# Optimization experiments

Hardware: AMD Instinct MI355X
Metric: run time of the kernel (lower is better)

## Reference

```python
import jax, jax.numpy as jnp
import numpy as np

N_HEADS = 16

def kernel_sigmoid(x):
    return jax.nn.sigmoid(0.6053 * x - 4.102)

def setup_inputs() -> dict:
    key = jax.random.key(0)
    kq, kk, kv = jax.random.split(key, 3)
    B, LQ, LK, E = 4, 4096, 4096, 1024
    return {
        "Q": jax.random.normal(kq, (B, LQ, E), dtype=jnp.float32),
        "K": jax.random.normal(kk, (B, LK, E), dtype=jnp.float32),
        "V": jax.random.normal(kv, (B, LK, E), dtype=jnp.float32),
    }

def reference(Q, K, V):
    B, LQ, E = Q.shape
    LK = K.shape[1]
    H = N_HEADS
    D = E // H
    # split heads -> [B, H, L, D]
    Qh = Q.reshape(B, LQ, H, D).transpose(0, 2, 1, 3)
    Kh = K.reshape(B, LK, H, D).transpose(0, 2, 1, 3)
    Vh = V.reshape(B, LK, H, D).transpose(0, 2, 1, 3)
    phi_Q = kernel_sigmoid(Qh)           # [B,H,LQ,D]
    phi_K = kernel_sigmoid(Kh)           # [B,H,LK,D]
    # KV state: phi_K^T @ V -> [B,H,D,D]
    kv = jnp.einsum("bhkd,bhke->bhde", phi_K, Vh)
    num = jnp.einsum("bhqd,bhde->bhqe", phi_Q, kv)      # [B,H,LQ,D]
    k_sum = phi_K.sum(axis=2)                            # [B,H,D]
    den = jnp.einsum("bhqd,bhd->bhq", phi_Q, k_sum)      # [B,H,LQ]
    out = num / den[..., None]
    # merge heads -> [B, LQ, E]
    return out.transpose(0, 2, 1, 3).reshape(B, LQ, E)
```

## Files before the change

kernel.cpp:

```cpp
#include <hip/hip_runtime.h>
#include <cstdint>
#include <cstddef>

#define B_ 4
#define L_ 4096
#define E_ 1024
#define H_ 16
#define D_ 64
#define BH_ 64
#define ST2_ 4160
#define NCH_ 16
#define RPC_ (L_/NCH_)
#define NT_ (RPC_/32)

typedef __attribute__((ext_vector_type(8))) short short8v;
typedef __attribute__((ext_vector_type(4))) float f32x4;

__device__ __forceinline__ float sigk(float x) {
    return __builtin_amdgcn_rcpf(1.0f + __expf(4.102f - 0.6053f * x));
}
__device__ __forceinline__ unsigned short bfh(float f) {
    union { float f; unsigned u; } v; v.f = f;
    const unsigned r = v.u + 0x7fffu + ((v.u >> 16) & 1u);
    return (unsigned short)(r >> 16);
}
__device__ __forceinline__ float bf2f(unsigned short s) {
    union { unsigned u; float f; } v; v.u = ((unsigned)s) << 16;
    return v.f;
}


__global__ void __launch_bounds__(256) kv_partial_kernel(
    const float* __restrict__ K, const float* __restrict__ V,
    float* __restrict__ partial)
{
    __shared__ short8v Bfrag[2 * 8 * 64];

    const int ch = blockIdx.x & (NCH_ - 1);
    const int bh = blockIdx.x / NCH_;
    const int b = bh >> 4, h = bh & 15;
    const int tid = threadIdx.x;
    const int w = tid >> 6, l = tid & 63;
    const int g = l >> 4, m = l & 15;
    const int k4 = g << 2;
    const int col = (w << 4) + m;

    const float* Kp = K + (size_t)(b * L_ + ch * RPC_) * E_ + h * D_ + col;
    const float* Vp = V + (size_t)(b * L_ + ch * RPC_) * E_ + h * D_ + col;

    f32x4 acc[4];
    #pragma unroll
    for (int t = 0; t < 4; ++t) acc[t] = (f32x4){0.f, 0.f, 0.f, 0.f};
    float ksacc = 0.f;

    float vr[8], kr[8];
    #pragma unroll
    for (int j = 0; j < 8; ++j) {
        const int ko = k4 + (j & 3) + ((j >> 2) << 4);
        vr[j] = Vp[(size_t)ko * E_];
        kr[j] = Kp[(size_t)ko * E_];
    }
    {
        short8v Bh, Bl;
        #pragma unroll
        for (int j = 0; j < 8; ++j) {
            const unsigned short hb = bfh(vr[j]);
            Bh[j] = (short)hb;
            Bl[j] = (short)bfh(vr[j] - bf2f(hb));
        }
        Bfrag[(w << 1) * 64 + l]       = Bh;
        Bfrag[((w << 1) + 1) * 64 + l] = Bl;
    }
    __syncthreads();

    #pragma unroll 2
    for (int t = 0; t < NT_; ++t) {
        const int buf = (t & 1) << 9;
        float vr2[8], kr2[8];
        if (t + 1 < NT_) {
            #pragma unroll
            for (int j = 0; j < 8; ++j) {
                const int ko = ((t + 1) << 5) + k4 + (j & 3) + ((j >> 2) << 4);
                vr2[j] = Vp[(size_t)ko * E_];
                kr2[j] = Kp[(size_t)ko * E_];
            }
        }
        short8v Ah;
        #pragma unroll
        for (int j = 0; j < 8; ++j) {
            const unsigned short hb = bfh(sigk(kr[j]));
            Ah[j] = (short)hb;
            ksacc += bf2f(hb);
        }
        #pragma unroll
        for (int tt = 0; tt < 4; ++tt) {
            const short8v Bh = Bfrag[buf + (tt << 1) * 64 + l];
            const short8v Bl = Bfrag[buf + ((tt << 1) + 1) * 64 + l];
            acc[tt] = __builtin_amdgcn_mfma_f32_16x16x32_bf16(Ah, Bh, acc[tt], 0, 0, 0);
            acc[tt] = __builtin_amdgcn_mfma_f32_16x16x32_bf16(Ah, Bl, acc[tt], 0, 0, 0);
        }
        if (t + 1 < NT_) {
            const int nbuf = ((t + 1) & 1) << 9;
            short8v Bh, Bl;
            #pragma unroll
            for (int j = 0; j < 8; ++j) {
                const unsigned short hb = bfh(vr2[j]);
                Bh[j] = (short)hb;
                Bl[j] = (short)bfh(vr2[j] - bf2f(hb));
            }
            Bfrag[nbuf + (w << 1) * 64 + l]       = Bh;
            Bfrag[nbuf + ((w << 1) + 1) * 64 + l] = Bl;
            #pragma unroll
            for (int j = 0; j < 8; ++j) kr[j] = kr2[j];
        }
        __syncthreads();
    }

    ksacc += __shfl_xor(ksacc, 16);
    ksacc += __shfl_xor(ksacc, 32);

    const size_t pbase = ((size_t)ch * BH_ + bh) * ST2_;
    #pragma unroll
    for (int tt = 0; tt < 4; ++tt)
        #pragma unroll
        for (int r = 0; r < 4; ++r)
            partial[pbase + (size_t)((w << 4) + k4 + r) * 64 + (tt << 4) + m]
                = acc[tt][r];
    if (g == 0) partial[pbase + 4096 + (w << 4) + m] = ksacc;
}

__global__ void __launch_bounds__(256) kv_reduce_kernel(
    const float* __restrict__ partial, unsigned* __restrict__ kv2,
    float* __restrict__ ksumf)
{
    const int bh = blockIdx.x >> 2, part = blockIdx.x & 3;
    const int tid = threadIdx.x;
    #pragma unroll
    for (int i = 0; i < 4; ++i) {
        const int idx = (part << 10) + (i << 8) + tid;
        float s = 0.f;
        #pragma unroll
        for (int c = 0; c < NCH_; ++c)
            s += partial[((size_t)c * BH_ + bh) * ST2_ + idx];
        const unsigned short hb = bfh(s);
        const unsigned short lb = bfh(s - bf2f(hb));
        kv2[(size_t)bh * 4096 + idx] = ((unsigned)hb << 16) | (unsigned)lb;
    }
    if (part == 0 && tid < 64) {
        float s = 0.f;
        #pragma unroll
        for (int c = 0; c < NCH_; ++c)
            s += partial[((size_t)c * BH_ + bh) * ST2_ + 4096 + tid];
        ksumf[bh * 64 + tid] = s;
    }
}

__global__ void __launch_bounds__(256) attn_out_kernel(
    const float* __restrict__ Q, const unsigned* __restrict__ kv2,
    const float* __restrict__ ksumf, float* __restrict__ out)
{
    __shared__ short8v fragBv[16 * 64];
    __shared__ float Qt[64 * 65];
    unsigned short* fragB = (unsigned short*)fragBv;

    const int bh = blockIdx.x >> 5, qb = blockIdx.x & 31;
    const int b = bh >> 4, h = bh & 15;
    const int tid = threadIdx.x;
    const int w = tid >> 6, l = tid & 63;
    const int g = l >> 4, m = l & 15;
    const int k4 = g << 2;

    #pragma unroll 4
    for (int i = 0; i < 16; ++i) {
        const int idx = tid + (i << 8);
        const unsigned u = kv2[(size_t)bh * 4096 + idx];
        const int dd = idx >> 6, e = idx & 63;
        const int kk = dd & 31, kstep = dd >> 5;
        const int gg = (kk & 15) >> 2;
        const int jj = (kk & 3) + ((kk >> 4) << 2);
        const int lane = (e & 15) + (gg << 4);
        const int tt2 = e >> 4;
        const int slot = (((kstep << 2) + tt2) << 1);
        fragB[(slot * 64 + lane) * 8 + jj]       = (unsigned short)(u >> 16);
        fragB[((slot + 1) * 64 + lane) * 8 + jj] = (unsigned short)(u & 0xffffu);
    }
    float ksl[16];
    #pragma unroll
    for (int ks = 0; ks < 2; ++ks)
        #pragma unroll
        for (int j = 0; j < 8; ++j)
            ksl[ks * 8 + j] =
                ksumf[bh * 64 + (ks << 5) + k4 + (j & 3) + ((j >> 2) << 4)];
    __syncthreads();

    for (int qt = 0; qt < 2; ++qt) {
        const int rowb0 = (qb << 7) + (qt << 6);
        #pragma unroll
        for (int i = 0; i < 4; ++i) {
            const int idx = tid + (i << 8);
            const int r = idx >> 4, c4i = (idx & 15) << 2;
            const float4 qv = *(const float4*)(
                Q + (size_t)(b * L_ + rowb0 + r) * E_ + h * D_ + c4i);
            float* qd = Qt + r * 65 + c4i;
            qd[0] = qv.x; qd[1] = qv.y; qd[2] = qv.z; qd[3] = qv.w;
        }
        __syncthreads();

        const int rl = (w << 4) + m;
        short8v Ah[2], Al[2];
        float den = 0.f;
        #pragma unroll
        for (int ks = 0; ks < 2; ++ks)
            #pragma unroll
            for (int j = 0; j < 8; ++j) {
                const float qv =
                    Qt[rl * 65 + (ks << 5) + k4 + (j & 3) + ((j >> 2) << 4)];
                const float ph = sigk(qv);
                const unsigned short hb = bfh(ph);
                Ah[ks][j] = (short)hb;
                Al[ks][j] = (short)bfh(ph - bf2f(hb));
                den = fmaf(ph, ksl[ks * 8 + j], den);
            }

        f32x4 acc[4];
        #pragma unroll
        for (int tt = 0; tt < 4; ++tt) acc[tt] = (f32x4){0.f, 0.f, 0.f, 0.f};
        #pragma unroll
        for (int ks = 0; ks < 2; ++ks)
            #pragma unroll
            for (int tt = 0; tt < 4; ++tt) {
                const int slot = (((ks << 2) + tt) << 1);
                const short8v Bh = fragBv[slot * 64 + l];
                const short8v Bl = fragBv[(slot + 1) * 64 + l];
                acc[tt] = __builtin_amdgcn_mfma_f32_16x16x32_bf16(Ah[ks], Bh, acc[tt], 0, 0, 0);
                acc[tt] = __builtin_amdgcn_mfma_f32_16x16x32_bf16(Ah[ks], Bl, acc[tt], 0, 0, 0);
                acc[tt] = __builtin_amdgcn_mfma_f32_16x16x32_bf16(Al[ks], Bh, acc[tt], 0, 0, 0);
            }

        den += __shfl_xor(den, 16);
        den += __shfl_xor(den, 32);
        float inv[4];
        #pragma unroll
        for (int r = 0; r < 4; ++r)
            inv[r] = __builtin_amdgcn_rcpf(__shfl(den, k4 + r));

        float* op = out + (size_t)(b * L_ + rowb0 + (w << 4)) * E_ + h * D_;
        #pragma unroll
        for (int tt = 0; tt < 4; ++tt)
            #pragma unroll
            for (int r = 0; r < 4; ++r)
                op[(size_t)(k4 + r) * E_ + (tt << 4) + m] = acc[tt][r] * inv[r];
        __syncthreads();
    }
}

extern "C" void kernel_launch(void* const* d_in, const int* in_sizes, int n_in,
                              void* d_out, int out_size, void* d_ws, size_t ws_size,
                              hipStream_t stream) {
    const float* Q = (const float*)d_in[0];
    const float* K = (const float*)d_in[1];
    const float* V = (const float*)d_in[2];
    float* out = (float*)d_out;

    float* partial  = (float*)d_ws;
    unsigned* kv2   = (unsigned*)(partial + (size_t)NCH_ * BH_ * ST2_);
    float* ksumf    = (float*)(kv2 + (size_t)BH_ * 4096);

    hipLaunchKernelGGL(kv_partial_kernel, dim3(BH_ * NCH_), dim3(256), 0, stream,
                       K, V, partial);
    hipLaunchKernelGGL(kv_reduce_kernel, dim3(BH_ * 4), dim3(256), 0, stream,
                       partial, kv2, ksumf);
    hipLaunchKernelGGL(attn_out_kernel, dim3(BH_ * 32), dim3(256), 0, stream,
                       Q, kv2, ksumf, out);
}
```

Before: 69.82 us.

## Raise KV chunk count, pre-swizzle KV fragments, one Q tile per block

The KV partial pass now splits each head into a runtime-chosen chunk count, up to 32 and capped by workspace size, to raise parallelism. The reduce kernel writes the hi/lo bf16 KV state directly in MFMA fragment order, so the output kernel can copy it into LDS with plain loads. The output kernel handles one 64-row Q tile per block with twice as many blocks, and precomputes the sigmoid and bf16 split of Q while staging it. The costs are more partial traffic in the reduce and more redundant KV staging across the extra output blocks.

```diff
diff --git a/kernel.cpp b/kernel.cpp
--- a/kernel.cpp
+++ b/kernel.cpp
@@ -9,9 +9,6 @@
 #define D_ 64
 #define BH_ 64
 #define ST2_ 4160
-#define NCH_ 16
-#define RPC_ (L_/NCH_)
-#define NT_ (RPC_/32)
 
 typedef __attribute__((ext_vector_type(8))) short short8v;
 typedef __attribute__((ext_vector_type(4))) float f32x4;
@@ -32,12 +29,12 @@
 
 __global__ void __launch_bounds__(256) kv_partial_kernel(
     const float* __restrict__ K, const float* __restrict__ V,
-    float* __restrict__ partial)
+    float* __restrict__ partial, int nch, int rowsPerCh, int nt)
 {
     __shared__ short8v Bfrag[2 * 8 * 64];
 
-    const int ch = blockIdx.x & (NCH_ - 1);
-    const int bh = blockIdx.x / NCH_;
+    const int ch = blockIdx.x % nch;
+    const int bh = blockIdx.x / nch;
     const int b = bh >> 4, h = bh & 15;
     const int tid = threadIdx.x;
     const int w = tid >> 6, l = tid & 63;
@@ -45,8 +42,8 @@
     const int k4 = g << 2;
     const int col = (w << 4) + m;
 
-    const float* Kp = K + (size_t)(b * L_ + ch * RPC_) * E_ + h * D_ + col;
-    const float* Vp = V + (size_t)(b * L_ + ch * RPC_) * E_ + h * D_ + col;
+    const float* Kp = K + (size_t)(b * L_ + ch * rowsPerCh) * E_ + h * D_ + col;
+    const float* Vp = V + (size_t)(b * L_ + ch * rowsPerCh) * E_ + h * D_ + col;
 
     f32x4 acc[4];
     #pragma unroll
@@ -74,10 +71,10 @@
     __syncthreads();
 
     #pragma unroll 2
-    for (int t = 0; t < NT_; ++t) {
+    for (int t = 0; t < nt; ++t) {
         const int buf = (t & 1) << 9;
         float vr2[8], kr2[8];
-        if (t + 1 < NT_) {
+        if (t + 1 < nt) {
             #pragma unroll
             for (int j = 0; j < 8; ++j) {
                 const int ko = ((t + 1) << 5) + k4 + (j & 3) + ((j >> 2) << 4);
@@ -99,7 +96,7 @@
             acc[tt] = __builtin_amdgcn_mfma_f32_16x16x32_bf16(Ah, Bh, acc[tt], 0, 0, 0);
             acc[tt] = __builtin_amdgcn_mfma_f32_16x16x32_bf16(Ah, Bl, acc[tt], 0, 0, 0);
         }
-        if (t + 1 < NT_) {
+        if (t + 1 < nt) {
             const int nbuf = ((t + 1) & 1) << 9;
             short8v Bh, Bl;
             #pragma unroll
@@ -131,7 +128,7 @@
 
 __global__ void __launch_bounds__(256) kv_reduce_kernel(
     const float* __restrict__ partial, unsigned* __restrict__ kv2,
-    float* __restrict__ ksumf)
+    float* __restrict__ ksumf, int nch)
 {
     const int bh = blockIdx.x >> 2, part = blockIdx.x & 3;
     const int tid = threadIdx.x;
@@ -139,17 +136,22 @@
     for (int i = 0; i < 4; ++i) {
         const int idx = (part << 10) + (i << 8) + tid;
         float s = 0.f;
-        #pragma unroll
-        for (int c = 0; c < NCH_; ++c)
+        for (int c = 0; c < nch; ++c)
             s += partial[((size_t)c * BH_ + bh) * ST2_ + idx];
         const unsigned short hb = bfh(s);
         const unsigned short lb = bfh(s - bf2f(hb));
-        kv2[(size_t)bh * 4096 + idx] = ((unsigned)hb << 16) | (unsigned)lb;
+        const unsigned u = ((unsigned)hb << 16) | (unsigned)lb;
+        const int d = idx >> 6, e = idx & 63;
+        const int kk = d & 31;
+        const int gg = (kk & 15) >> 2;
+        const int jj = (kk & 3) + ((kk >> 4) << 2);
+        const int lane = (e & 15) + (gg << 4);
+        const int sp = ((d >> 5) << 2) + (e >> 4);
+        kv2[(size_t)bh * 4096 + ((sp << 6) + lane) * 8 + jj] = u;
     }
     if (part == 0 && tid < 64) {
         float s = 0.f;
-        #pragma unroll
-        for (int c = 0; c < NCH_; ++c)
+        for (int c = 0; c < nch; ++c)
             s += partial[((size_t)c * BH_ + bh) * ST2_ + 4096 + tid];
         ksumf[bh * 64 + tid] = s;
     }
@@ -159,99 +161,106 @@
     const float* __restrict__ Q, const unsigned* __restrict__ kv2,
     const float* __restrict__ ksumf, float* __restrict__ out)
 {
-    __shared__ short8v fragBv[16 * 64];
-    __shared__ float Qt[64 * 65];
-    unsigned short* fragB = (unsigned short*)fragBv;
-
-    const int bh = blockIdx.x >> 5, qb = blockIdx.x & 31;
+    __shared__ unsigned kvf[4096];
+    __shared__ uint4 QA4[1024];
+
+    const int bh = blockIdx.x >> 6, qb = blockIdx.x & 63;
     const int b = bh >> 4, h = bh & 15;
     const int tid = threadIdx.x;
     const int w = tid >> 6, l = tid & 63;
     const int g = l >> 4, m = l & 15;
     const int k4 = g << 2;
-
-    #pragma unroll 4
-    for (int i = 0; i < 16; ++i) {
+    const int rowb0 = qb << 6;
+
+    #pragma unroll
+    for (int i = 0; i < 16; ++i)
+        kvf[tid + (i << 8)] = kv2[(size_t)bh * 4096 + tid + (i << 8)];
+
+    #pragma unroll
+    for (int i = 0; i < 4; ++i) {
         const int idx = tid + (i << 8);
-        const unsigned u = kv2[(size_t)bh * 4096 + idx];
-        const int dd = idx >> 6, e = idx & 63;
-        const int kk = dd & 31, kstep = dd >> 5;
-        const int gg = (kk & 15) >> 2;
-        const int jj = (kk & 3) + ((kk >> 4) << 2);
-        const int lane = (e & 15) + (gg << 4);
-        const int tt2 = e >> 4;
-        const int slot = (((kstep << 2) + tt2) << 1);
-        fragB[(slot * 64 + lane) * 8 + jj]       = (unsigned short)(u >> 16);
-        fragB[((slot + 1) * 64 + lane) * 8 + jj] = (unsigned short)(u & 0xffffu);
-    }
+        const int r = idx >> 4;
+        const int c4i = (idx & 15) << 2;
+        const float4 qv = *(const float4*)(
+            Q + (size_t)(b * L_ + rowb0 + r) * E_ + h * D_ + c4i);
+        const float qa[4] = {qv.x, qv.y, qv.z, qv.w};
+        unsigned u[4];
+        #pragma unroll
+        for (int j = 0; j < 4; ++j) {
+            const float ph = sigk(qa[j]);
+            const unsigned short hb = bfh(ph);
+            const unsigned short lb = bfh(ph - bf2f(hb));
+            u[j] = ((unsigned)hb << 16) | (unsigned)lb;
+        }
+        const int lane = (tid >> 4) + ((tid & 3) << 4);
+        const int qq = (tid >> 2) & 3;
+        QA4[(((qq << 2) + i) << 6) + lane] = make_uint4(u[0], u[1], u[2], u[3]);
+    }
+
     float ksl[16];
     #pragma unroll
+    for (int ji = 0; ji < 16; ++ji) {
+        const int ks = ji >> 3, j = ji & 7;
+        ksl[ji] = ksumf[bh * 64 + (ks << 5) + k4 + (j & 3) + ((j >> 2) << 4)];
+    }
+    __syncthreads();
+
+    const uint4 aq0 = QA4[((0 << 2) + w) * 64 + l];
+    const uint4 aq1 = QA4[((1 << 2) + w) * 64 + l];
+    const uint4 aq2 = QA4[((2 << 2) + w) * 64 + l];
+    const uint4 aq3 = QA4[((3 << 2) + w) * 64 + l];
+    const unsigned au[16] = {aq0.x, aq0.y, aq0.z, aq0.w,
+                             aq1.x, aq1.y, aq1.z, aq1.w,
+                             aq2.x, aq2.y, aq2.z, aq2.w,
+                             aq3.x, aq3.y, aq3.z, aq3.w};
+    short8v Ah[2], Al[2];
+    float den = 0.f;
+    #pragma unroll
+    for (int ji = 0; ji < 16; ++ji) {
+        const unsigned uu = au[ji];
+        const unsigned short hb = (unsigned short)(uu >> 16);
+        const unsigned short lb = (unsigned short)(uu & 0xffffu);
+        Ah[ji >> 3][ji & 7] = (short)hb;
+        Al[ji >> 3][ji & 7] = (short)lb;
+        den = fmaf(bf2f(hb) + bf2f(lb), ksl[ji], den);
+    }
+
+    f32x4 acc[4];
+    #pragma unroll
+    for (int tt = 0; tt < 4; ++tt) acc[tt] = (f32x4){0.f, 0.f, 0.f, 0.f};
+    #pragma unroll
     for (int ks = 0; ks < 2; ++ks)
         #pragma unroll
-        for (int j = 0; j < 8; ++j)
-            ksl[ks * 8 + j] =
-                ksumf[bh * 64 + (ks << 5) + k4 + (j & 3) + ((j >> 2) << 4)];
-    __syncthreads();
-
-    for (int qt = 0; qt < 2; ++qt) {
-        const int rowb0 = (qb << 7) + (qt << 6);
-        #pragma unroll
-        for (int i = 0; i < 4; ++i) {
-            const int idx = tid + (i << 8);
-            const int r = idx >> 4, c4i = (idx & 15) << 2;
-            const float4 qv = *(const float4*)(
-                Q + (size_t)(b * L_ + rowb0 + r) * E_ + h * D_ + c4i);
-            float* qd = Qt + r * 65 + c4i;
-            qd[0] = qv.x; qd[1] = qv.y; qd[2] = qv.z; qd[3] = qv.w;
-        }
-        __syncthreads();
-
-        const int rl = (w << 4) + m;
-        short8v Ah[2], Al[2];
-        float den = 0.f;
-        #pragma unroll
-        for (int ks = 0; ks < 2; ++ks)
+        for (int tt = 0; tt < 4; ++tt) {
+            const int base = ((((ks << 2) + tt) << 6) + l) << 3;
+            const uint4 b0 = *(const uint4*)&kvf[base];
+            const uint4 b1 = *(const uint4*)&kvf[base + 4];
+            const unsigned bu[8] = {b0.x, b0.y, b0.z, b0.w,
+                                    b1.x, b1.y, b1.z, b1.w};
+            short8v Bh, Bl;
             #pragma unroll
             for (int j = 0; j < 8; ++j) {
-                const float qv =
-                    Qt[rl * 65 + (ks << 5) + k4 + (j & 3) + ((j >> 2) << 4)];
-                const float ph = sigk(qv);
-                const unsigned short hb = bfh(ph);
-                Ah[ks][j] = (short)hb;
-                Al[ks][j] = (short)bfh(ph - bf2f(hb));
-                den = fmaf(ph, ksl[ks * 8 + j], den);
+                Bh[j] = (short)(bu[j] >> 16);
+                Bl[j] = (short)(bu[j] & 0xffffu);
             }
-
-        f32x4 acc[4];
-        #pragma unroll
-        for (int tt = 0; tt < 4; ++tt) acc[tt] = (f32x4){0.f, 0.f, 0.f, 0.f};
-        #pragma unroll
-        for (int ks = 0; ks < 2; ++ks)
-            #pragma unroll
-            for (int tt = 0; tt < 4; ++tt) {
-                const int slot = (((ks << 2) + tt) << 1);
-                const short8v Bh = fragBv[slot * 64 + l];
-                const short8v Bl = fragBv[(slot + 1) * 64 + l];
-                acc[tt] = __builtin_amdgcn_mfma_f32_16x16x32_bf16(Ah[ks], Bh, acc[tt], 0, 0, 0);
-                acc[tt] = __builtin_amdgcn_mfma_f32_16x16x32_bf16(Ah[ks], Bl, acc[tt], 0, 0, 0);
-                acc[tt] = __builtin_amdgcn_mfma_f32_16x16x32_bf16(Al[ks], Bh, acc[tt], 0, 0, 0);
-            }
-
-        den += __shfl_xor(den, 16);
-        den += __shfl_xor(den, 32);
-        float inv[4];
+            acc[tt] = __builtin_amdgcn_mfma_f32_16x16x32_bf16(Ah[ks], Bh, acc[tt], 0, 0, 0);
+            acc[tt] = __builtin_amdgcn_mfma_f32_16x16x32_bf16(Ah[ks], Bl, acc[tt], 0, 0, 0);
+            acc[tt] = __builtin_amdgcn_mfma_f32_16x16x32_bf16(Al[ks], Bh, acc[tt], 0, 0, 0);
+        }
+
+    den += __shfl_xor(den, 16);
+    den += __shfl_xor(den, 32);
+    float inv[4];
+    #pragma unroll
+    for (int r = 0; r < 4; ++r)
+        inv[r] = __builtin_amdgcn_rcpf(__shfl(den, k4 + r));
+
+    float* op = out + (size_t)(b * L_ + rowb0 + (w << 4)) * E_ + h * D_;
+    #pragma unroll
+    for (int tt = 0; tt < 4; ++tt)
         #pragma unroll
         for (int r = 0; r < 4; ++r)
-            inv[r] = __builtin_amdgcn_rcpf(__shfl(den, k4 + r));
-
-        float* op = out + (size_t)(b * L_ + rowb0 + (w << 4)) * E_ + h * D_;
-        #pragma unroll
-        for (int tt = 0; tt < 4; ++tt)
-            #pragma unroll
-            for (int r = 0; r < 4; ++r)
-                op[(size_t)(k4 + r) * E_ + (tt << 4) + m] = acc[tt][r] * inv[r];
-        __syncthreads();
-    }
+            op[(size_t)(k4 + r) * E_ + (tt << 4) + m] = acc[tt][r] * inv[r];
 }
 
 extern "C" void kernel_launch(void* const* d_in, const int* in_sizes, int n_in,
@@ -262,14 +271,22 @@
     const float* V = (const float*)d_in[2];
     float* out = (float*)d_out;
 
+    int nch = 32;
+    while (nch > 4 &&
+           (size_t)nch * BH_ * ST2_ * 4 + (size_t)BH_ * 4096 * 4 + BH_ * 64 * 4
+               > ws_size)
+        nch >>= 1;
+    const int rowsPerCh = L_ / nch;
+    const int nt = rowsPerCh / 32;
+
     float* partial  = (float*)d_ws;
-    unsigned* kv2   = (unsigned*)(partial + (size_t)NCH_ * BH_ * ST2_);
+    unsigned* kv2   = (unsigned*)(partial + (size_t)nch * BH_ * ST2_);
     float* ksumf    = (float*)(kv2 + (size_t)BH_ * 4096);
 
-    hipLaunchKernelGGL(kv_partial_kernel, dim3(BH_ * NCH_), dim3(256), 0, stream,
-                       K, V, partial);
+    hipLaunchKernelGGL(kv_partial_kernel, dim3(BH_ * nch), dim3(256), 0, stream,
+                       K, V, partial, nch, rowsPerCh, nt);
     hipLaunchKernelGGL(kv_reduce_kernel, dim3(BH_ * 4), dim3(256), 0, stream,
-                       partial, kv2, ksumf);
-    hipLaunchKernelGGL(attn_out_kernel, dim3(BH_ * 32), dim3(256), 0, stream,
+                       partial, kv2, ksumf, nch);
+    hipLaunchKernelGGL(attn_out_kernel, dim3(BH_ * 64), dim3(256), 0, stream,
                        Q, kv2, ksumf, out);
 }
```

Result: slower. 110.6 us (+58.5%).

## Pre-swizzle KV state into MFMA fragment layout and deepen K/V prefetch

Applied to the files above, without the earlier changes.

The reduce kernel now writes the KV state as separate hi/lo bf16 arrays already arranged in MFMA B-fragment order. The output kernel can then copy it to shared memory with straight vector loads instead of a scattered 16-bit shuffle. The output kernel handles one 64-row query tile per block with twice as many blocks, which removes its loop and the extra barriers. The partial kernel prefetches K/V two tiles ahead and adds a scheduling barrier. The denominator now uses the bf16-split phi value, and the extra register and register-to-shared traffic may add pressure.

```diff
diff --git a/kernel.cpp b/kernel.cpp
--- a/kernel.cpp
+++ b/kernel.cpp
@@ -53,65 +53,72 @@
     for (int t = 0; t < 4; ++t) acc[t] = (f32x4){0.f, 0.f, 0.f, 0.f};
     float ksacc = 0.f;
 
-    float vr[8], kr[8];
+    float kr[2][8], vr[2][8];
     #pragma unroll
     for (int j = 0; j < 8; ++j) {
         const int ko = k4 + (j & 3) + ((j >> 2) << 4);
-        vr[j] = Vp[(size_t)ko * E_];
-        kr[j] = Kp[(size_t)ko * E_];
+        kr[0][j] = Kp[(size_t)ko * E_];
+        vr[0][j] = Vp[(size_t)ko * E_];
     }
     {
         short8v Bh, Bl;
         #pragma unroll
         for (int j = 0; j < 8; ++j) {
-            const unsigned short hb = bfh(vr[j]);
+            const unsigned short hb = bfh(vr[0][j]);
             Bh[j] = (short)hb;
-            Bl[j] = (short)bfh(vr[j] - bf2f(hb));
+            Bl[j] = (short)bfh(vr[0][j] - bf2f(hb));
         }
         Bfrag[(w << 1) * 64 + l]       = Bh;
         Bfrag[((w << 1) + 1) * 64 + l] = Bl;
     }
+    #pragma unroll
+    for (int j = 0; j < 8; ++j) {
+        const int ko = 32 + k4 + (j & 3) + ((j >> 2) << 4);
+        kr[1][j] = Kp[(size_t)ko * E_];
+        vr[1][j] = Vp[(size_t)ko * E_];
+    }
     __syncthreads();
 
     #pragma unroll 2
     for (int t = 0; t < NT_; ++t) {
-        const int buf = (t & 1) << 9;
-        float vr2[8], kr2[8];
-        if (t + 1 < NT_) {
+        const int cur = t & 1, nxt = cur ^ 1;
+        short8v Ah;
+        #pragma unroll
+        for (int j = 0; j < 8; ++j) {
+            const unsigned short hb = bfh(sigk(kr[cur][j]));
+            Ah[j] = (short)hb;
+            ksacc += bf2f(hb);
+        }
+        if (t + 2 < NT_) {
             #pragma unroll
             for (int j = 0; j < 8; ++j) {
-                const int ko = ((t + 1) << 5) + k4 + (j & 3) + ((j >> 2) << 4);
-                vr2[j] = Vp[(size_t)ko * E_];
-                kr2[j] = Kp[(size_t)ko * E_];
+                const int ko = ((t + 2) << 5) + k4 + (j & 3) + ((j >> 2) << 4);
+                kr[cur][j] = Kp[(size_t)ko * E_];
+                vr[cur][j] = Vp[(size_t)ko * E_];
             }
         }
-        short8v Ah;
-        #pragma unroll
-        for (int j = 0; j < 8; ++j) {
-            const unsigned short hb = bfh(sigk(kr[j]));
-            Ah[j] = (short)hb;
-            ksacc += bf2f(hb);
-        }
-        #pragma unroll
-        for (int tt = 0; tt < 4; ++tt) {
-            const short8v Bh = Bfrag[buf + (tt << 1) * 64 + l];
-            const short8v Bl = Bfrag[buf + ((tt << 1) + 1) * 64 + l];
-            acc[tt] = __builtin_amdgcn_mfma_f32_16x16x32_bf16(Ah, Bh, acc[tt], 0, 0, 0);
-            acc[tt] = __builtin_amdgcn_mfma_f32_16x16x32_bf16(Ah, Bl, acc[tt], 0, 0, 0);
+        __builtin_amdgcn_sched_barrier(0);
+        {
+            const int buf = cur << 9;
+            #pragma unroll
+            for (int tt = 0; tt < 4; ++tt) {
+                const short8v Bh = Bfrag[buf + (tt << 1) * 64 + l];
+                const short8v Bl = Bfrag[buf + ((tt << 1) + 1) * 64 + l];
+                acc[tt] = __builtin_amdgcn_mfma_f32_16x16x32_bf16(Ah, Bh, acc[tt], 0, 0, 0);
+                acc[tt] = __builtin_amdgcn_mfma_f32_16x16x32_bf16(Ah, Bl, acc[tt], 0, 0, 0);
+            }
         }
         if (t + 1 < NT_) {
-            const int nbuf = ((t + 1) & 1) << 9;
+            const int nb = nxt << 9;
             short8v Bh, Bl;
             #pragma unroll
             for (int j = 0; j < 8; ++j) {
-                const unsigned short hb = bfh(vr2[j]);
+                const unsigned short hb = bfh(vr[nxt][j]);
                 Bh[j] = (short)hb;
-                Bl[j] = (short)bfh(vr2[j] - bf2f(hb));
+                Bl[j] = (short)bfh(vr[nxt][j] - bf2f(hb));
             }
-            Bfrag[nbuf + (w << 1) * 64 + l]       = Bh;
-            Bfrag[nbuf + ((w << 1) + 1) * 64 + l] = Bl;
-            #pragma unroll
-            for (int j = 0; j < 8; ++j) kr[j] = kr2[j];
+            Bfrag[nb + (w << 1) * 64 + l]       = Bh;
+            Bfrag[nb + ((w << 1) + 1) * 64 + l] = Bl;
         }
         __syncthreads();
     }
@@ -130,21 +137,34 @@
 }
 
 __global__ void __launch_bounds__(256) kv_reduce_kernel(
-    const float* __restrict__ partial, unsigned* __restrict__ kv2,
-    float* __restrict__ ksumf)
+    const float* __restrict__ partial, unsigned* __restrict__ kv2H,
+    unsigned* __restrict__ kv2L, float* __restrict__ ksumf)
 {
     const int bh = blockIdx.x >> 2, part = blockIdx.x & 3;
     const int tid = threadIdx.x;
-    #pragma unroll
-    for (int i = 0; i < 4; ++i) {
-        const int idx = (part << 10) + (i << 8) + tid;
-        float s = 0.f;
-        #pragma unroll
-        for (int c = 0; c < NCH_; ++c)
-            s += partial[((size_t)c * BH_ + bh) * ST2_ + idx];
-        const unsigned short hb = bfh(s);
-        const unsigned short lb = bfh(s - bf2f(hb));
-        kv2[(size_t)bh * 4096 + idx] = ((unsigned)hb << 16) | (unsigned)lb;
+    const int e = tid & 63;
+    #pragma unroll
+    for (int it = 0; it < 2; ++it) {
+        const int pr = (tid >> 6) + (it << 2);
+        const int d0 = (part << 4) + (pr << 1);
+        float s0 = 0.f, s1 = 0.f;
+        #pragma unroll
+        for (int c = 0; c < NCH_; ++c) {
+            const size_t pb = ((size_t)c * BH_ + bh) * ST2_;
+            s0 += partial[pb + (d0 << 6) + e];
+            s1 += partial[pb + ((d0 + 1) << 6) + e];
+        }
+        const unsigned short h0 = bfh(s0), h1 = bfh(s1);
+        const unsigned short l0 = bfh(s0 - bf2f(h0));
+        const unsigned short l1 = bfh(s1 - bf2f(h1));
+        const int kk = d0 & 31;
+        const int gg = (kk & 15) >> 2;
+        const int jq = ((kk & 3) >> 1) + ((kk >> 4) << 1);
+        const int lane = (e & 15) + (gg << 4);
+        const int sp = ((d0 >> 5) << 2) + (e >> 4);
+        const size_t idx = (size_t)bh * 2048 + (((sp << 6) + lane) << 2) + jq;
+        kv2H[idx] = (unsigned)h0 | ((unsigned)h1 << 16);
+        kv2L[idx] = (unsigned)l0 | ((unsigned)l1 << 16);
     }
     if (part == 0 && tid < 64) {
         float s = 0.f;
@@ -156,102 +176,94 @@
 }
 
 __global__ void __launch_bounds__(256) attn_out_kernel(
-    const float* __restrict__ Q, const unsigned* __restrict__ kv2,
-    const float* __restrict__ ksumf, float* __restrict__ out)
+    const float* __restrict__ Q, const unsigned* __restrict__ kv2H,
+    const unsigned* __restrict__ kv2L, const float* __restrict__ ksumf,
+    float* __restrict__ out)
 {
-    __shared__ short8v fragBv[16 * 64];
+    __shared__ short8v kvH[8 * 64];
+    __shared__ short8v kvL[8 * 64];
     __shared__ float Qt[64 * 65];
-    unsigned short* fragB = (unsigned short*)fragBv;
-
-    const int bh = blockIdx.x >> 5, qb = blockIdx.x & 31;
+
+    const int bh = blockIdx.x >> 6, qb = blockIdx.x & 63;
     const int b = bh >> 4, h = bh & 15;
     const int tid = threadIdx.x;
     const int w = tid >> 6, l = tid & 63;
     const int g = l >> 4, m = l & 15;
     const int k4 = g << 2;
-
-    #pragma unroll 4
-    for (int i = 0; i < 16; ++i) {
+    const int rowb0 = qb << 6;
+
+    {
+        const uint4* srcH = (const uint4*)(kv2H + (size_t)bh * 2048);
+        const uint4* srcL = (const uint4*)(kv2L + (size_t)bh * 2048);
+        uint4* dH = (uint4*)kvH;
+        uint4* dL = (uint4*)kvL;
+        dH[tid]       = srcH[tid];
+        dH[tid + 256] = srcH[tid + 256];
+        dL[tid]       = srcL[tid];
+        dL[tid + 256] = srcL[tid + 256];
+    }
+    #pragma unroll
+    for (int i = 0; i < 4; ++i) {
         const int idx = tid + (i << 8);
-        const unsigned u = kv2[(size_t)bh * 4096 + idx];
-        const int dd = idx >> 6, e = idx & 63;
-        const int kk = dd & 31, kstep = dd >> 5;
-        const int gg = (kk & 15) >> 2;
-        const int jj = (kk & 3) + ((kk >> 4) << 2);
-        const int lane = (e & 15) + (gg << 4);
-        const int tt2 = e >> 4;
-        const int slot = (((kstep << 2) + tt2) << 1);
-        fragB[(slot * 64 + lane) * 8 + jj]       = (unsigned short)(u >> 16);
-        fragB[((slot + 1) * 64 + lane) * 8 + jj] = (unsigned short)(u & 0xffffu);
+        const int r = idx >> 4, c4i = (idx & 15) << 2;
+        const float4 qv = *(const float4*)(
+            Q + (size_t)(b * L_ + rowb0 + r) * E_ + h * D_ + c4i);
+        float* qd = Qt + r * 65 + c4i;
+        qd[0] = qv.x; qd[1] = qv.y; qd[2] = qv.z; qd[3] = qv.w;
     }
     float ksl[16];
     #pragma unroll
+    for (int ji = 0; ji < 16; ++ji) {
+        const int ks = ji >> 3, j = ji & 7;
+        ksl[ji] = ksumf[bh * 64 + (ks << 5) + k4 + (j & 3) + ((j >> 2) << 4)];
+    }
+    __syncthreads();
+
+    const int rl = (w << 4) + m;
+    short8v Ah[2], Al[2];
+    float den = 0.f;
+    #pragma unroll
     for (int ks = 0; ks < 2; ++ks)
         #pragma unroll
-        for (int j = 0; j < 8; ++j)
-            ksl[ks * 8 + j] =
-                ksumf[bh * 64 + (ks << 5) + k4 + (j & 3) + ((j >> 2) << 4)];
-    __syncthreads();
-
-    for (int qt = 0; qt < 2; ++qt) {
-        const int rowb0 = (qb << 7) + (qt << 6);
-        #pragma unroll
-        for (int i = 0; i < 4; ++i) {
-            const int idx = tid + (i << 8);
-            const int r = idx >> 4, c4i = (idx & 15) << 2;
-            const float4 qv = *(const float4*)(
-                Q + (size_t)(b * L_ + rowb0 + r) * E_ + h * D_ + c4i);
-            float* qd = Qt + r * 65 + c4i;
-            qd[0] = qv.x; qd[1] = qv.y; qd[2] = qv.z; qd[3] = qv.w;
-        }
-        __syncthreads();
-
-        const int rl = (w << 4) + m;
-        short8v Ah[2], Al[2];
-        float den = 0.f;
-        #pragma unroll
-        for (int ks = 0; ks < 2; ++ks)
-            #pragma unroll
-            for (int j = 0; j < 8; ++j) {
-                const float qv =
-                    Qt[rl * 65 + (ks << 5) + k4 + (j & 3) + ((j >> 2) << 4)];
-                const float ph = sigk(qv);
-                const unsigned short hb = bfh(ph);
-                Ah[ks][j] = (short)hb;
-                Al[ks][j] = (short)bfh(ph - bf2f(hb));
-                den = fmaf(ph, ksl[ks * 8 + j], den);
-            }
-
-        f32x4 acc[4];
-        #pragma unroll
-        for (int tt = 0; tt < 4; ++tt) acc[tt] = (f32x4){0.f, 0.f, 0.f, 0.f};
-        #pragma unroll
-        for (int ks = 0; ks < 2; ++ks)
-            #pragma unroll
-            for (int tt = 0; tt < 4; ++tt) {
-                const int slot = (((ks << 2) + tt) << 1);
-                const short8v Bh = fragBv[slot * 64 + l];
-                const short8v Bl = fragBv[(slot + 1) * 64 + l];
-                acc[tt] = __builtin_amdgcn_mfma_f32_16x16x32_bf16(Ah[ks], Bh, acc[tt], 0, 0, 0);
-                acc[tt] = __builtin_amdgcn_mfma_f32_16x16x32_bf16(Ah[ks], Bl, acc[tt], 0, 0, 0);
-                acc[tt] = __builtin_amdgcn_mfma_f32_16x16x32_bf16(Al[ks], Bh, acc[tt], 0, 0, 0);
-            }
-
-        den += __shfl_xor(den, 16);
-        den += __shfl_xor(den, 32);
-        float inv[4];
+        for (int j = 0; j < 8; ++j) {
+            const float qv =
+                Qt[rl * 65 + (ks << 5) + k4 + (j & 3) + ((j >> 2) << 4)];
+            const float ph = sigk(qv);
+            const unsigned short hb = bfh(ph);
+            const unsigned short lb = bfh(ph - bf2f(hb));
+            Ah[ks][j] = (short)hb;
+            Al[ks][j] = (short)lb;
+            den = fmaf(bf2f(hb) + bf2f(lb), ksl[(ks << 3) + j], den);
+        }
+
+    f32x4 acc[4];
+    #pragma unroll
+    for (int tt = 0; tt < 4; ++tt) acc[tt] = (f32x4){0.f, 0.f, 0.f, 0.f};
+    #pragma unroll
+    for (int ks = 0; ks < 2; ++ks)
+        #pragma unroll
+        for (int tt = 0; tt < 4; ++tt) {
+            const int slot = (ks << 2) + tt;
+            const short8v Bh = kvH[slot * 64 + l];
+            const short8v Bl = kvL[slot * 64 + l];
+            acc[tt] = __builtin_amdgcn_mfma_f32_16x16x32_bf16(Ah[ks], Bh, acc[tt], 0, 0, 0);
+            acc[tt] = __builtin_amdgcn_mfma_f32_16x16x32_bf16(Ah[ks], Bl, acc[tt], 0, 0, 0);
+            acc[tt] = __builtin_amdgcn_mfma_f32_16x16x32_bf16(Al[ks], Bh, acc[tt], 0, 0, 0);
+        }
+
+    den += __shfl_xor(den, 16);
+    den += __shfl_xor(den, 32);
+    float inv[4];
+    #pragma unroll
+    for (int r = 0; r < 4; ++r)
+        inv[r] = __builtin_amdgcn_rcpf(__shfl(den, k4 + r));
+
+    float* op = out + (size_t)(b * L_ + rowb0 + (w << 4)) * E_ + h * D_;
+    #pragma unroll
+    for (int tt = 0; tt < 4; ++tt)
         #pragma unroll
         for (int r = 0; r < 4; ++r)
-            inv[r] = __builtin_amdgcn_rcpf(__shfl(den, k4 + r));
-
-        float* op = out + (size_t)(b * L_ + rowb0 + (w << 4)) * E_ + h * D_;
-        #pragma unroll
-        for (int tt = 0; tt < 4; ++tt)
-            #pragma unroll
-            for (int r = 0; r < 4; ++r)
-                op[(size_t)(k4 + r) * E_ + (tt << 4) + m] = acc[tt][r] * inv[r];
-        __syncthreads();
-    }
+            op[(size_t)(k4 + r) * E_ + (tt << 4) + m] = acc[tt][r] * inv[r];
 }
 
 extern "C" void kernel_launch(void* const* d_in, const int* in_sizes, int n_in,
@@ -262,14 +274,15 @@
     const float* V = (const float*)d_in[2];
     float* out = (float*)d_out;
 
-    float* partial  = (float*)d_ws;
-    unsigned* kv2   = (unsigned*)(partial + (size_t)NCH_ * BH_ * ST2_);
-    float* ksumf    = (float*)(kv2 + (size_t)BH_ * 4096);
+    float* partial = (float*)d_ws;
+    unsigned* kv2H = (unsigned*)(partial + (size_t)NCH_ * BH_ * ST2_);
+    unsigned* kv2L = kv2H + (size_t)BH_ * 2048;
+    float* ksumf   = (float*)(kv2L + (size_t)BH_ * 2048);
 
     hipLaunchKernelGGL(kv_partial_kernel, dim3(BH_ * NCH_), dim3(256), 0, stream,
                        K, V, partial);
     hipLaunchKernelGGL(kv_reduce_kernel, dim3(BH_ * 4), dim3(256), 0, stream,
-                       partial, kv2, ksumf);
-    hipLaunchKernelGGL(attn_out_kernel, dim3(BH_ * 32), dim3(256), 0, stream,
-                       Q, kv2, ksumf, out);
-}
+                       partial, kv2H, kv2L, ksumf);
+    hipLaunchKernelGGL(attn_out_kernel, dim3(BH_ * 64), dim3(256), 0, stream,
+                       Q, kv2H, kv2L, ksumf, out);
+}
```

New measurement: 67.42 us. -3.4%, faster.
